# Kernel optimization log

Measured on AMD Instinct MI355X. Metric: run time of the kernel, lower is better.

Reference implementation:

```python
import jax, jax.numpy as jnp
import numpy as np

N = 50000
E = 800000
IN, HID, OUT = 256, 128, 64
NEG_SLOPE = 0.2


def _gat(x, src, dst, W, a_src, a_dst, b, heads, dim, concat):
    # PyG GATConv (eval mode, self-loops already appended to src/dst)
    xh = (x @ W).reshape(N, heads, dim)              # [N,H,D]
    s_src = jnp.einsum('nhd,hd->nh', xh, a_src)       # [N,H]
    s_dst = jnp.einsum('nhd,hd->nh', xh, a_dst)
    e = jax.nn.leaky_relu(s_src[src] + s_dst[dst], NEG_SLOPE)  # [Etot,H]
    m = jax.ops.segment_max(e, dst, num_segments=N)
    e = jnp.exp(e - m[dst])
    z = jax.ops.segment_sum(e, dst, num_segments=N)
    alpha = e / z[dst]                                # segment softmax over incoming edges
    msg = xh[src] * alpha[:, :, None]                 # [Etot,H,D] gather + weight
    out = jax.ops.segment_sum(msg, dst, num_segments=N)  # scatter-add aggregate
    out = out.reshape(N, heads * dim) if concat else out.mean(axis=1)
    return out + b


def setup_inputs():
    key = jax.random.key(0)
    ks = jax.random.split(key, 20)
    sc = 0.05
    inp = {
        'x': jax.random.normal(ks[0], (N, IN), jnp.float32),
        'edge_index': jax.random.randint(ks[1], (2, E), 0, N, jnp.int64) if jax.config.read('jax_enable_x64') else jax.random.randint(ks[1], (2, E), 0, N, jnp.int32),
        # semantic MLP
        'w1': jax.random.normal(ks[2], (IN, HID), jnp.float32) * sc,
        'b1': jnp.zeros((HID,), jnp.float32),
        'w2': jax.random.normal(ks[3], (HID, HID), jnp.float32) * sc,
        'b2': jnp.zeros((HID,), jnp.float32),
        # gat1: HID -> HID//2, heads=4, concat -> 2*HID
        'g1_w': jax.random.normal(ks[4], (HID, 4 * (HID // 2)), jnp.float32) * sc,
        'g1_asrc': jax.random.normal(ks[5], (4, HID // 2), jnp.float32) * sc,
        'g1_adst': jax.random.normal(ks[6], (4, HID // 2), jnp.float32) * sc,
        'g1_b': jnp.zeros((2 * HID,), jnp.float32),
        # gat2: 2*HID -> OUT, heads=2, mean
        'g2_w': jax.random.normal(ks[7], (2 * HID, 2 * OUT), jnp.float32) * sc,
        'g2_asrc': jax.random.normal(ks[8], (2, OUT), jnp.float32) * sc,
        'g2_adst': jax.random.normal(ks[9], (2, OUT), jnp.float32) * sc,
        'g2_b': jnp.zeros((OUT,), jnp.float32),
        # gat3: OUT -> OUT, heads=1, mean
        'g3_w': jax.random.normal(ks[10], (OUT, OUT), jnp.float32) * sc,
        'g3_asrc': jax.random.normal(ks[11], (1, OUT), jnp.float32) * sc,
        'g3_adst': jax.random.normal(ks[12], (1, OUT), jnp.float32) * sc,
        'g3_b': jnp.zeros((OUT,), jnp.float32),
    }
    return inp


def reference(x, edge_index, w1, b1, w2, b2,
              g1_w, g1_asrc, g1_adst, g1_b,
              g2_w, g2_asrc, g2_adst, g2_b,
              g3_w, g3_asrc, g3_adst, g3_b):
    # add self loops once (PyG GATConv default add_self_loops=True)
    loop = jnp.arange(N, dtype=edge_index.dtype)
    src = jnp.concatenate([edge_index[0], loop])
    dst = jnp.concatenate([edge_index[1], loop])
    # semantic MLP (eval: dropout is identity)
    h = jax.nn.relu(x @ w1 + b1)
    h = jax.nn.relu(h @ w2 + b2)
    h = jax.nn.elu(_gat(h, src, dst, g1_w, g1_asrc, g1_adst, g1_b, 4, HID // 2, True))
    h = jax.nn.elu(_gat(h, src, dst, g2_w, g2_asrc, g2_adst, g2_b, 2, OUT, False))
    h = _gat(h, src, dst, g3_w, g3_asrc, g3_adst, g3_b, 1, OUT, False)
    return h
```

## Files before the change

kernel.cpp:

```cpp
#include <hip/hip_runtime.h>
#include <hip/hip_fp16.h>
#include <math.h>

#define NN 50000
#define NE 800000

static inline int ceil_div_h(int a, int b) { return (a + b - 1) / b; }

typedef _Float16 half8 __attribute__((ext_vector_type(8)));
typedef float f32x4 __attribute__((ext_vector_type(4)));

__global__ __launch_bounds__(256)
void prep_kernel(const float* __restrict__ w1, const float* __restrict__ w2,
                 const float* __restrict__ g1w, const float* __restrict__ g2w,
                 const float* __restrict__ g3w, __half* __restrict__ wt,
                 int* __restrict__ cursor) {
  int idx = blockIdx.x * 256 + threadIdx.x;
  if (idx < NN) cursor[idx] = 0;
  const float* W; int K, N, li;
  if (idx < 32768)        { W = w1;  K = 256; N = 128; li = idx; }
  else if (idx < 49152)   { W = w2;  K = 128; N = 128; li = idx - 32768; }
  else if (idx < 81920)   { W = g1w; K = 128; N = 256; li = idx - 49152; }
  else if (idx < 114688)  { W = g2w; K = 256; N = 128; li = idx - 81920; }
  else if (idx < 118784)  { W = g3w; K = 64;  N = 64;  li = idx - 114688; }
  else return;
  int n = li / K, k = li - n * K;
  wt[idx] = __float2half_rn(W[(size_t)k * N + n]);
}

__global__ __launch_bounds__(256)
void mlp_gat1_fused(const float* __restrict__ x,
                    const __half* __restrict__ wt1,
                    const float* __restrict__ b1,
                    const __half* __restrict__ wt2,
                    const float* __restrict__ b2,
                    const __half* __restrict__ wtg1,
                    const float* __restrict__ a_src, const float* __restrict__ a_dst,
                    __half* __restrict__ xh1,
                    float* __restrict__ s_src, float* __restrict__ s_dst) {
  constexpr int SA = 40;
  constexpr int SH = 136;
  __shared__ __align__(16) _Float16 As[64 * SA];
  __shared__ __align__(16) _Float16 Bs[256 * SA];
  __shared__ __align__(16) _Float16 h1s[64 * SH];
  __shared__ __align__(16) _Float16 h2s[64 * SH];
  const int tid = threadIdx.x;
  const int bm = blockIdx.x * 64;
  const int wave = tid >> 6, lane = tid & 63;
  const int l16 = lane & 15, quad = lane >> 4;
  const int wm = (wave & 1) * 32;
  const int wn = (wave >> 1) * 64;

  {
    f32x4 acc[2][4] = {};
    for (int k0 = 0; k0 < 256; k0 += 32) {
      #pragma unroll
      for (int i = 0; i < 2; ++i) {
        int idx = tid + i * 256;
        int m = idx >> 3, q = idx & 7;
        int gm = bm + m;
        float4 v = make_float4(0.f, 0.f, 0.f, 0.f);
        if (gm < NN) v = *(const float4*)&x[(size_t)gm * 256 + k0 + q * 4];
        union { __half2 h2[2]; float2 f2; } u;
        u.h2[0] = __floats2half2_rn(v.x, v.y);
        u.h2[1] = __floats2half2_rn(v.z, v.w);
        *(float2*)&As[m * SA + q * 4] = u.f2;
      }
      #pragma unroll
      for (int i = 0; i < 2; ++i) {
        int idx = tid + i * 256;
        int n = idx >> 2, kq = (idx & 3) * 8;
        *(float4*)&Bs[n * SA + kq] = *(const float4*)&wt1[(size_t)n * 256 + k0 + kq];
      }
      __syncthreads();
      half8 af[2], bf[4];
      #pragma unroll
      for (int mi = 0; mi < 2; ++mi)
        af[mi] = *(const half8*)&As[(wm + mi * 16 + l16) * SA + quad * 8];
      #pragma unroll
      for (int ni = 0; ni < 4; ++ni)
        bf[ni] = *(const half8*)&Bs[(wn + ni * 16 + l16) * SA + quad * 8];
      #pragma unroll
      for (int mi = 0; mi < 2; ++mi)
        #pragma unroll
        for (int ni = 0; ni < 4; ++ni)
          acc[mi][ni] = __builtin_amdgcn_mfma_f32_16x16x32_f16(af[mi], bf[ni], acc[mi][ni], 0, 0, 0);
      __syncthreads();
    }
    #pragma unroll
    for (int mi = 0; mi < 2; ++mi)
      #pragma unroll
      for (int r = 0; r < 4; ++r) {
        int row = wm + mi * 16 + quad * 4 + r;
        #pragma unroll
        for (int ni = 0; ni < 4; ++ni) {
          int col = wn + ni * 16 + l16;
          float v = acc[mi][ni][r] + b1[col];
          v = fmaxf(v, 0.f);
          h1s[row * SH + col] = (_Float16)v;
        }
      }
  }
  __syncthreads();

  {
    f32x4 acc[2][4] = {};
    for (int k0 = 0; k0 < 128; k0 += 32) {
      #pragma unroll
      for (int i = 0; i < 2; ++i) {
        int idx = tid + i * 256;
        int n = idx >> 2, kq = (idx & 3) * 8;
        *(float4*)&Bs[n * SA + kq] = *(const float4*)&wt2[(size_t)n * 128 + k0 + kq];
      }
      __syncthreads();
      half8 af[2], bf[4];
      #pragma unroll
      for (int mi = 0; mi < 2; ++mi)
        af[mi] = *(const half8*)&h1s[(wm + mi * 16 + l16) * SH + k0 + quad * 8];
      #pragma unroll
      for (int ni = 0; ni < 4; ++ni)
        bf[ni] = *(const half8*)&Bs[(wn + ni * 16 + l16) * SA + quad * 8];
      #pragma unroll
      for (int mi = 0; mi < 2; ++mi)
        #pragma unroll
        for (int ni = 0; ni < 4; ++ni)
          acc[mi][ni] = __builtin_amdgcn_mfma_f32_16x16x32_f16(af[mi], bf[ni], acc[mi][ni], 0, 0, 0);
      __syncthreads();
    }
    #pragma unroll
    for (int mi = 0; mi < 2; ++mi)
      #pragma unroll
      for (int r = 0; r < 4; ++r) {
        int row = wm + mi * 16 + quad * 4 + r;
        #pragma unroll
        for (int ni = 0; ni < 4; ++ni) {
          int col = wn + ni * 16 + l16;
          float v = acc[mi][ni][r] + b2[col];
          v = fmaxf(v, 0.f);
          h2s[row * SH + col] = (_Float16)v;
        }
      }
  }
  __syncthreads();

  {
    f32x4 acc[4][4] = {};
    const int wn3 = wave * 64;
    for (int k0 = 0; k0 < 128; k0 += 32) {
      #pragma unroll
      for (int i = 0; i < 4; ++i) {
        int idx = tid + i * 256;
        int n = idx >> 2, kq = (idx & 3) * 8;
        *(float4*)&Bs[n * SA + kq] = *(const float4*)&wtg1[(size_t)n * 128 + k0 + kq];
      }
      __syncthreads();
      half8 af[4], bf[4];
      #pragma unroll
      for (int mi = 0; mi < 4; ++mi)
        af[mi] = *(const half8*)&h2s[(mi * 16 + l16) * SH + k0 + quad * 8];
      #pragma unroll
      for (int ni = 0; ni < 4; ++ni)
        bf[ni] = *(const half8*)&Bs[(wn3 + ni * 16 + l16) * SA + quad * 8];
      #pragma unroll
      for (int mi = 0; mi < 4; ++mi)
        #pragma unroll
        for (int ni = 0; ni < 4; ++ni)
          acc[mi][ni] = __builtin_amdgcn_mfma_f32_16x16x32_f16(af[mi], bf[ni], acc[mi][ni], 0, 0, 0);
      __syncthreads();
    }
    float asv[4], adv[4];
    #pragma unroll
    for (int ni = 0; ni < 4; ++ni) {
      int d = ni * 16 + l16;
      asv[ni] = a_src[wave * 64 + d];
      adv[ni] = a_dst[wave * 64 + d];
    }
    #pragma unroll
    for (int mi = 0; mi < 4; ++mi) {
      #pragma unroll
      for (int r = 0; r < 4; ++r) {
        int gm = bm + mi * 16 + quad * 4 + r;
        float ss = 0.f, sd = 0.f;
        #pragma unroll
        for (int ni = 0; ni < 4; ++ni) {
          float v = acc[mi][ni][r];
          ss = fmaf(v, asv[ni], ss);
          sd = fmaf(v, adv[ni], sd);
          if (gm < NN) xh1[(size_t)gm * 256 + wn3 + ni * 16 + l16] = __float2half_rn(v);
        }
        #pragma unroll
        for (int off = 1; off < 16; off <<= 1) {
          ss += __shfl_xor(ss, off, 64);
          sd += __shfl_xor(sd, off, 64);
        }
        if (l16 == 0 && gm < NN) {
          s_src[gm * 4 + wave] = ss;
          s_dst[gm * 4 + wave] = sd;
        }
      }
    }
  }
}

template<int BM, int TN, int WR, int WC, int ACT, int OUTH, int AF32, int HS>
__global__ __launch_bounds__(256)
void mfma_gemm(const void* __restrict__ Av, const __half* __restrict__ Bt,
               const float* __restrict__ bias, void* __restrict__ Cv,
               const float* __restrict__ a_src, const float* __restrict__ a_dst,
               float* __restrict__ s_src, float* __restrict__ s_dst,
               int M, int N, int K) {
  constexpr int FM = BM / WR / 16;
  constexpr int FN = TN / WC / 16;
  constexpr int SA = 40;
  __shared__ __align__(16) _Float16 As[BM * SA];
  __shared__ __align__(16) _Float16 Bs[TN * SA];
  const int tid = threadIdx.x;
  const int bm = blockIdx.y * BM, bn = blockIdx.x * TN;
  const int wave = tid >> 6, lane = tid & 63;
  const int wm = (wave % WR) * (BM / WR);
  const int wn = (wave / WR) * (TN / WC);
  const int l16 = lane & 15, quad = lane >> 4;

  f32x4 acc[FM][FN] = {};

  for (int k0 = 0; k0 < K; k0 += 32) {
    if (AF32) {
      const float* A = (const float*)Av;
      #pragma unroll
      for (int i = 0; i < (BM * 8) / 256; ++i) {
        int idx = tid + i * 256;
        int m = idx >> 3, q = idx & 7;
        int gm = bm + m;
        float4 v = make_float4(0.f, 0.f, 0.f, 0.f);
        if (gm < M) v = *(const float4*)&A[(size_t)gm * K + k0 + q * 4];
        union { __half2 h2[2]; float2 f2; } u;
        u.h2[0] = __floats2half2_rn(v.x, v.y);
        u.h2[1] = __floats2half2_rn(v.z, v.w);
        *(float2*)&As[m * SA + q * 4] = u.f2;
      }
    } else {
      const __half* A = (const __half*)Av;
      #pragma unroll
      for (int i = 0; i < (BM * 4) / 256; ++i) {
        int idx = tid + i * 256;
        int m = idx >> 2, q = (idx & 3) * 8;
        int gm = bm + m;
        float4 raw = make_float4(0.f, 0.f, 0.f, 0.f);
        if (gm < M) raw = *(const float4*)&A[(size_t)gm * K + k0 + q];
        *(float4*)&As[m * SA + q] = raw;
      }
    }
    #pragma unroll
    for (int i = 0; i < (TN * 4) / 256; ++i) {
      int idx = tid + i * 256;
      int n = idx >> 2, kq = (idx & 3) * 8;
      float4 raw = *(const float4*)&Bt[(size_t)(bn + n) * K + k0 + kq];
      *(float4*)&Bs[n * SA + kq] = raw;
    }
    __syncthreads();
    half8 af[FM], bf[FN];
    #pragma unroll
    for (int mi = 0; mi < FM; ++mi)
      af[mi] = *(const half8*)&As[(wm + mi * 16 + l16) * SA + quad * 8];
    #pragma unroll
    for (int ni = 0; ni < FN; ++ni)
      bf[ni] = *(const half8*)&Bs[(wn + ni * 16 + l16) * SA + quad * 8];
    #pragma unroll
    for (int mi = 0; mi < FM; ++mi)
      #pragma unroll
      for (int ni = 0; ni < FN; ++ni)
        acc[mi][ni] = __builtin_amdgcn_mfma_f32_16x16x32_f16(af[mi], bf[ni], acc[mi][ni], 0, 0, 0);
    __syncthreads();
  }

  #pragma unroll
  for (int mi = 0; mi < FM; ++mi) {
    #pragma unroll
    for (int r = 0; r < 4; ++r) {
      int gm = bm + wm + mi * 16 + quad * 4 + r;
      if (gm >= M) continue;
      #pragma unroll
      for (int ni = 0; ni < FN; ++ni) {
        int gn = bn + wn + ni * 16 + l16;
        float v = acc[mi][ni][r];
        if (bias) v += bias[gn];
        if (ACT == 1) v = fmaxf(v, 0.f);
        if (OUTH) ((__half*)Cv)[(size_t)gm * N + gn] = __float2half_rn(v);
        else      ((float*)Cv)[(size_t)gm * N + gn] = v;
      }
    }
  }

  if (HS > 0) {
    const int h = (bn + wn) >> 6;
    float asv[FN], adv[FN];
    #pragma unroll
    for (int ni = 0; ni < FN; ++ni) {
      int d = ni * 16 + l16;
      asv[ni] = a_src[h * 64 + d];
      adv[ni] = a_dst[h * 64 + d];
    }
    #pragma unroll
    for (int mi = 0; mi < FM; ++mi) {
      #pragma unroll
      for (int r = 0; r < 4; ++r) {
        float ss = 0.f, sd = 0.f;
        #pragma unroll
        for (int ni = 0; ni < FN; ++ni) {
          float v = acc[mi][ni][r];
          ss = fmaf(v, asv[ni], ss);
          sd = fmaf(v, adv[ni], sd);
        }
        #pragma unroll
        for (int off = 1; off < 16; off <<= 1) {
          ss += __shfl_xor(ss, off, 64);
          sd += __shfl_xor(sd, off, 64);
        }
        int gm = bm + wm + mi * 16 + quad * 4 + r;
        if (l16 == 0 && gm < M) {
          s_src[gm * HS + h] = ss;
          s_dst[gm * HS + h] = sd;
        }
      }
    }
  }
}


__global__ __launch_bounds__(256)
void hist_kernel(const int* __restrict__ ei, int* __restrict__ cnt) {
  int e = blockIdx.x * blockDim.x + threadIdx.x;
  if (e >= NE) return;
  atomicAdd(&cnt[ei[NE + e]], 1);
}

__global__ __launch_bounds__(256)
void scan1_kernel(const int* __restrict__ in, int* __restrict__ out,
                  int* __restrict__ bsum, int n) {
  __shared__ int tmp[256];
  int t = threadIdx.x;
  int i = blockIdx.x * 256 + t;
  int v = (i < n) ? in[i] : 0;
  tmp[t] = v;
  __syncthreads();
  for (int off = 1; off < 256; off <<= 1) {
    int u = (t >= off) ? tmp[t - off] : 0;
    __syncthreads();
    tmp[t] += u;
    __syncthreads();
  }
  if (i <= n) out[i] = tmp[t] - v;
  if (t == 255) bsum[blockIdx.x] = tmp[255];
}

__global__ __launch_bounds__(256)
void scan2_kernel(int* __restrict__ data, int n) {
  __shared__ int tmp[256];
  int t = threadIdx.x;
  int v = (t < n) ? data[t] : 0;
  tmp[t] = v;
  __syncthreads();
  for (int off = 1; off < 256; off <<= 1) {
    int u = (t >= off) ? tmp[t - off] : 0;
    __syncthreads();
    tmp[t] += u;
    __syncthreads();
  }
  if (t < n) data[t] = tmp[t] - v;
}

__global__ __launch_bounds__(256)
void scan3_kernel(int* __restrict__ out, const int* __restrict__ bsum,
                  int* __restrict__ cursor, int n) {
  int i = blockIdx.x * 256 + threadIdx.x;
  if (i > n) return;
  int v = out[i] + bsum[blockIdx.x];
  out[i] = v;
  if (i < n) cursor[i] = v;
}

__global__ __launch_bounds__(256)
void scatter_kernel(const int* __restrict__ ei, int* __restrict__ cursor,
                    int* __restrict__ srcs) {
  int e = blockIdx.x * blockDim.x + threadIdx.x;
  if (e >= NE) return;
  int s = ei[e], d = ei[NE + e];
  int pos = atomicAdd(&cursor[d], 1);
  srcs[pos] = s;
}

template<int H, int MODE>
__global__ __launch_bounds__(256)
void gat_aggregate(const int* __restrict__ rowptr, const int* __restrict__ srcs,
                   const float* __restrict__ ssrc, const float* __restrict__ sdst,
                   const __half* __restrict__ xh, const float* __restrict__ bias,
                   void* __restrict__ outv) {
  constexpr int HD = H * 64;
  __shared__ float wbuf[4][64 * H];
  __shared__ int sbuf[4][64];
  const int wslot = threadIdx.x >> 6;
  const int wid = (blockIdx.x * blockDim.x + threadIdx.x) >> 6;
  const int lane = threadIdx.x & 63;
  if (wid >= NN) return;
  const int n = wid;
  const int start = rowptr[n];
  const int end = rowptr[n + 1];
  const int h = (lane * H) >> 6;

  float sdv[H];
  #pragma unroll
  for (int hh = 0; hh < H; ++hh) sdv[hh] = sdst[n * H + hh];

  float z;
  float acc[H];
  {
    float wself[H];
    #pragma unroll
    for (int hh = 0; hh < H; ++hh) {
      float e = ssrc[n * H + hh] + sdv[hh];
      e = e >= 0.f ? e : 0.2f * e;
      wself[hh] = __expf(e);
    }
    float ws = wself[h];
    z = ws;
    const __half* xr = xh + (size_t)n * HD + lane * H;
    if (H == 4) {
      float2 raw = *(const float2*)xr;
      __half2 p0 = *(__half2*)&raw.x;
      __half2 p1 = *(__half2*)&raw.y;
      float2 f0 = __half22float2(p0), f1 = __half22float2(p1);
      acc[0] = ws * f0.x; acc[1] = ws * f0.y; acc[2] = ws * f1.x; acc[3] = ws * f1.y;
    } else if (H == 2) {
      float2 f0 = __half22float2(*(const __half2*)xr);
      acc[0] = ws * f0.x; acc[1] = ws * f0.y;
    } else {
      acc[0] = ws * __half2float(xr[0]);
    }
  }

  for (int base = start; base < end; base += 64) {
    int cnt = end - base;
    if (cnt > 64) cnt = 64;
    if (lane < cnt) {
      int s = srcs[base + lane];
      sbuf[wslot][lane] = s;
      float ev[H];
      if (H == 4) {
        float4 t = *(const float4*)&ssrc[s * 4];
        ev[0] = t.x; ev[1] = t.y; ev[2] = t.z; ev[3] = t.w;
      } else if (H == 2) {
        float2 t = *(const float2*)&ssrc[s * 2];
        ev[0] = t.x; ev[1] = t.y;
      } else {
        ev[0] = ssrc[s];
      }
      #pragma unroll
      for (int hh = 0; hh < H; ++hh) {
        float e = ev[hh] + sdv[hh];
        e = e >= 0.f ? e : 0.2f * e;
        wbuf[wslot][lane * H + hh] = __expf(e);
      }
    }
    #pragma unroll 4
    for (int j = 0; j < cnt; ++j) {
      int s = sbuf[wslot][j];
      float w = wbuf[wslot][j * H + h];
      z += w;
      const __half* xr = xh + (size_t)s * HD + lane * H;
      if (H == 4) {
        float2 raw = *(const float2*)xr;
        __half2 p0 = *(__half2*)&raw.x;
        __half2 p1 = *(__half2*)&raw.y;
        float2 f0 = __half22float2(p0), f1 = __half22float2(p1);
        acc[0] = fmaf(w, f0.x, acc[0]); acc[1] = fmaf(w, f0.y, acc[1]);
        acc[2] = fmaf(w, f1.x, acc[2]); acc[3] = fmaf(w, f1.y, acc[3]);
      } else if (H == 2) {
        float2 f0 = __half22float2(*(const __half2*)xr);
        acc[0] = fmaf(w, f0.x, acc[0]); acc[1] = fmaf(w, f0.y, acc[1]);
      } else {
        acc[0] = fmaf(w, __half2float(xr[0]), acc[0]);
      }
    }
  }
  const float inv = 1.f / z;

  if (MODE == 0) {
    __half* out = (__half*)outv;
    float v[4];
    #pragma unroll
    for (int i = 0; i < 4; ++i) {
      v[i] = acc[i] * inv + bias[lane * 4 + i];
      v[i] = v[i] > 0.f ? v[i] : expm1f(v[i]);
    }
    union { __half2 h2[2]; float2 f2; } u;
    u.h2[0] = __floats2half2_rn(v[0], v[1]);
    u.h2[1] = __floats2half2_rn(v[2], v[3]);
    *(float2*)&out[(size_t)n * 256 + lane * 4] = u.f2;
  } else if (MODE == 1) {
    __half* out = (__half*)outv;
    float sv[2];
    #pragma unroll
    for (int i = 0; i < 2; ++i) {
      float mine = acc[i] * inv;
      float other = __shfl_xor(mine, 32, 64);
      sv[i] = (mine + other) * 0.5f;
    }
    if (lane < 32) {
      float v0 = sv[0] + bias[lane * 2 + 0];
      float v1 = sv[1] + bias[lane * 2 + 1];
      v0 = v0 > 0.f ? v0 : expm1f(v0);
      v1 = v1 > 0.f ? v1 : expm1f(v1);
      *(__half2*)&out[(size_t)n * 64 + lane * 2] = __floats2half2_rn(v0, v1);
    }
  } else {
    float* out = (float*)outv;
    out[(size_t)n * 64 + lane] = acc[0] * inv + bias[lane];
  }
}


extern "C" void kernel_launch(void* const* d_in, const int* in_sizes, int n_in,
                              void* d_out, int out_size, void* d_ws, size_t ws_size,
                              hipStream_t stream) {
  const float* x    = (const float*)d_in[0];
  const int*   ei   = (const int*)d_in[1];
  const float* w1   = (const float*)d_in[2];
  const float* b1   = (const float*)d_in[3];
  const float* w2   = (const float*)d_in[4];
  const float* b2   = (const float*)d_in[5];
  const float* g1w  = (const float*)d_in[6];
  const float* g1as = (const float*)d_in[7];
  const float* g1ad = (const float*)d_in[8];
  const float* g1b  = (const float*)d_in[9];
  const float* g2w  = (const float*)d_in[10];
  const float* g2as = (const float*)d_in[11];
  const float* g2ad = (const float*)d_in[12];
  const float* g2b  = (const float*)d_in[13];
  const float* g3w  = (const float*)d_in[14];
  const float* g3as = (const float*)d_in[15];
  const float* g3ad = (const float*)d_in[16];
  const float* g3b  = (const float*)d_in[17];
  float* out = (float*)d_out;

  float* ws   = (float*)d_ws;
  float* bufA = ws;
  float* bufB = bufA + (size_t)NN * 256;
  float* bufC = bufB + (size_t)NN * 256;
  float* ssrc = bufC + (size_t)NN * 256;
  float* sdst = ssrc + (size_t)NN * 4;
  int* rowptr = (int*)(sdst + (size_t)NN * 4);
  int* cursor = rowptr + (NN + 1);
  int* bsum   = cursor + NN;
  int* srcs   = bsum + 256;
  __half* wt   = (__half*)(srcs + NE);
  __half* wt1  = wt;
  __half* wt2  = wt + 32768;
  __half* wtg1 = wt + 49152;
  __half* wtg2 = wt + 81920;
  __half* wtg3 = wt + 114688;

  __half* xh1 = (__half*)bufC;
  __half* a1  = (__half*)bufA;
  __half* xh2 = (__half*)bufB;
  __half* a2  = (__half*)bufC;
  __half* xh3 = (__half*)bufB;

  const int TB = 256;
  const int grid_m = ceil_div_h(NN, 64);
  const int egrid = ceil_div_h(NE, TB);
  const int sgrid = ceil_div_h(NN + 1, TB);
  const int wgrid = ceil_div_h(NN, 4);

  prep_kernel<<<ceil_div_h(118784, TB), TB, 0, stream>>>(w1, w2, g1w, g2w, g3w, wt, cursor);

  hist_kernel<<<egrid, TB, 0, stream>>>(ei, cursor);
  scan1_kernel<<<sgrid, TB, 0, stream>>>(cursor, rowptr, bsum, NN);
  scan2_kernel<<<1, TB, 0, stream>>>(bsum, sgrid);
  scan3_kernel<<<sgrid, TB, 0, stream>>>(rowptr, bsum, cursor, NN);
  scatter_kernel<<<egrid, TB, 0, stream>>>(ei, cursor, srcs);

  mlp_gat1_fused<<<grid_m, TB, 0, stream>>>(x, wt1, b1, wt2, b2, wtg1,
                                            g1as, g1ad, xh1, ssrc, sdst);
  gat_aggregate<4, 0><<<wgrid, TB, 0, stream>>>(rowptr, srcs, ssrc, sdst, xh1, g1b, a1);

  mfma_gemm<64, 128, 2, 2, 0, 1, 0, 2><<<dim3(1, grid_m), TB, 0, stream>>>(
      a1, wtg2, nullptr, xh2, g2as, g2ad, ssrc, sdst, NN, 128, 256);
  gat_aggregate<2, 1><<<wgrid, TB, 0, stream>>>(rowptr, srcs, ssrc, sdst, xh2, g2b, a2);

  mfma_gemm<64, 64, 4, 1, 0, 1, 0, 1><<<dim3(1, grid_m), TB, 0, stream>>>(
      a2, wtg3, nullptr, xh3, g3as, g3ad, ssrc, sdst, NN, 64, 64);
  gat_aggregate<1, 2><<<wgrid, TB, 0, stream>>>(rowptr, srcs, ssrc, sdst, xh3, g3b, out);
}
```

Baseline: 407.1 us.

## Fuse CSR build and weight prep into one cooperative kernel with grid syncs

Replaces the separate prep, histogram, three-pass scan and scatter launches with a single cooperative kernel of 196 blocks that uses grid.sync between phases. This removes five kernel launches and their inter-kernel gaps. In exchange, the edge-parallel atomic phases now run on far fewer blocks with grid-stride loops, and the cooperative launch adds its own overhead. The fused MLP kernel also reuses one shared-memory region for the B tiles, cutting its LDS footprint, which may raise occupancy.

```diff
diff --git a/kernel.cpp b/kernel.cpp
--- a/kernel.cpp
+++ b/kernel.cpp
@@ -1,31 +1,89 @@
 #include <hip/hip_runtime.h>
 #include <hip/hip_fp16.h>
+#include <hip/hip_cooperative_groups.h>
 #include <math.h>
 
 #define NN 50000
 #define NE 800000
 
+namespace cg = cooperative_groups;
+
 static inline int ceil_div_h(int a, int b) { return (a + b - 1) / b; }
 
 typedef _Float16 half8 __attribute__((ext_vector_type(8)));
 typedef float f32x4 __attribute__((ext_vector_type(4)));
 
 __global__ __launch_bounds__(256)
-void prep_kernel(const float* __restrict__ w1, const float* __restrict__ w2,
-                 const float* __restrict__ g1w, const float* __restrict__ g2w,
-                 const float* __restrict__ g3w, __half* __restrict__ wt,
-                 int* __restrict__ cursor) {
-  int idx = blockIdx.x * 256 + threadIdx.x;
-  if (idx < NN) cursor[idx] = 0;
-  const float* W; int K, N, li;
-  if (idx < 32768)        { W = w1;  K = 256; N = 128; li = idx; }
-  else if (idx < 49152)   { W = w2;  K = 128; N = 128; li = idx - 32768; }
-  else if (idx < 81920)   { W = g1w; K = 128; N = 256; li = idx - 49152; }
-  else if (idx < 114688)  { W = g2w; K = 256; N = 128; li = idx - 81920; }
-  else if (idx < 118784)  { W = g3w; K = 64;  N = 64;  li = idx - 114688; }
-  else return;
-  int n = li / K, k = li - n * K;
-  wt[idx] = __float2half_rn(W[(size_t)k * N + n]);
+void build_all_kernel(const float* __restrict__ w1, const float* __restrict__ w2,
+                      const float* __restrict__ g1w, const float* __restrict__ g2w,
+                      const float* __restrict__ g3w, __half* __restrict__ wt,
+                      const int* __restrict__ ei, int* __restrict__ cursor,
+                      int* __restrict__ rowptr, int* __restrict__ bsum,
+                      int* __restrict__ srcs) {
+  cg::grid_group grid = cg::this_grid();
+  const int tid = threadIdx.x;
+  const int gidx = blockIdx.x * 256 + tid;
+  const int gsz = gridDim.x * 256;
+  __shared__ int tmp[256];
+
+  if (gidx < NN) cursor[gidx] = 0;
+  for (int idx = gidx; idx < 118784; idx += gsz) {
+    const float* W; int K, N, li;
+    if (idx < 32768)        { W = w1;  K = 256; N = 128; li = idx; }
+    else if (idx < 49152)   { W = w2;  K = 128; N = 128; li = idx - 32768; }
+    else if (idx < 81920)   { W = g1w; K = 128; N = 256; li = idx - 49152; }
+    else if (idx < 114688)  { W = g2w; K = 256; N = 128; li = idx - 81920; }
+    else                    { W = g3w; K = 64;  N = 64;  li = idx - 114688; }
+    int n = li / K, k = li - n * K;
+    wt[idx] = __float2half_rn(W[(size_t)k * N + n]);
+  }
+  grid.sync();
+
+  for (int e = gidx; e < NE; e += gsz)
+    atomicAdd(&cursor[ei[NE + e]], 1);
+  grid.sync();
+
+  {
+    int v = (gidx < NN) ? cursor[gidx] : 0;
+    tmp[tid] = v;
+    __syncthreads();
+    for (int off = 1; off < 256; off <<= 1) {
+      int u = (tid >= off) ? tmp[tid - off] : 0;
+      __syncthreads();
+      tmp[tid] += u;
+      __syncthreads();
+    }
+    if (gidx <= NN) rowptr[gidx] = tmp[tid] - v;
+    if (tid == 255) bsum[blockIdx.x] = tmp[255];
+  }
+  grid.sync();
+
+  if (blockIdx.x == 0) {
+    int b = (tid < (int)gridDim.x) ? bsum[tid] : 0;
+    tmp[tid] = b;
+    __syncthreads();
+    for (int off = 1; off < 256; off <<= 1) {
+      int u = (tid >= off) ? tmp[tid - off] : 0;
+      __syncthreads();
+      tmp[tid] += u;
+      __syncthreads();
+    }
+    if (tid < (int)gridDim.x) bsum[tid] = tmp[tid] - b;
+  }
+  grid.sync();
+
+  if (gidx <= NN) {
+    int val = rowptr[gidx] + bsum[blockIdx.x];
+    rowptr[gidx] = val;
+    if (gidx < NN) cursor[gidx] = val;
+  }
+  grid.sync();
+
+  for (int e = gidx; e < NE; e += gsz) {
+    int s = ei[e], d = ei[NE + e];
+    int pos = atomicAdd(&cursor[d], 1);
+    srcs[pos] = s;
+  }
 }
 
 __global__ __launch_bounds__(256)
@@ -40,10 +98,12 @@
                     float* __restrict__ s_src, float* __restrict__ s_dst) {
   constexpr int SA = 40;
   constexpr int SH = 136;
-  __shared__ __align__(16) _Float16 As[64 * SA];
-  __shared__ __align__(16) _Float16 Bs[256 * SA];
-  __shared__ __align__(16) _Float16 h1s[64 * SH];
-  __shared__ __align__(16) _Float16 h2s[64 * SH];
+  __shared__ __align__(16) _Float16 smem[25088];
+  _Float16* As   = smem;
+  _Float16* Bs12 = smem + 2560;
+  _Float16* h1s  = smem + 7680;
+  _Float16* h2s  = smem + 16384;
+  _Float16* Bs3  = Bs12;
   const int tid = threadIdx.x;
   const int bm = blockIdx.x * 64;
   const int wave = tid >> 6, lane = tid & 63;
@@ -70,7 +130,7 @@
       for (int i = 0; i < 2; ++i) {
         int idx = tid + i * 256;
         int n = idx >> 2, kq = (idx & 3) * 8;
-        *(float4*)&Bs[n * SA + kq] = *(const float4*)&wt1[(size_t)n * 256 + k0 + kq];
+        *(float4*)&Bs12[n * SA + kq] = *(const float4*)&wt1[(size_t)n * 256 + k0 + kq];
       }
       __syncthreads();
       half8 af[2], bf[4];
@@ -79,7 +139,7 @@
         af[mi] = *(const half8*)&As[(wm + mi * 16 + l16) * SA + quad * 8];
       #pragma unroll
       for (int ni = 0; ni < 4; ++ni)
-        bf[ni] = *(const half8*)&Bs[(wn + ni * 16 + l16) * SA + quad * 8];
+        bf[ni] = *(const half8*)&Bs12[(wn + ni * 16 + l16) * SA + quad * 8];
       #pragma unroll
       for (int mi = 0; mi < 2; ++mi)
         #pragma unroll
@@ -110,7 +170,7 @@
       for (int i = 0; i < 2; ++i) {
         int idx = tid + i * 256;
         int n = idx >> 2, kq = (idx & 3) * 8;
-        *(float4*)&Bs[n * SA + kq] = *(const float4*)&wt2[(size_t)n * 128 + k0 + kq];
+        *(float4*)&Bs12[n * SA + kq] = *(const float4*)&wt2[(size_t)n * 128 + k0 + kq];
       }
       __syncthreads();
       half8 af[2], bf[4];
@@ -119,7 +179,7 @@
         af[mi] = *(const half8*)&h1s[(wm + mi * 16 + l16) * SH + k0 + quad * 8];
       #pragma unroll
       for (int ni = 0; ni < 4; ++ni)
-        bf[ni] = *(const half8*)&Bs[(wn + ni * 16 + l16) * SA + quad * 8];
+        bf[ni] = *(const half8*)&Bs12[(wn + ni * 16 + l16) * SA + quad * 8];
       #pragma unroll
       for (int mi = 0; mi < 2; ++mi)
         #pragma unroll
@@ -151,7 +211,7 @@
       for (int i = 0; i < 4; ++i) {
         int idx = tid + i * 256;
         int n = idx >> 2, kq = (idx & 3) * 8;
-        *(float4*)&Bs[n * SA + kq] = *(const float4*)&wtg1[(size_t)n * 128 + k0 + kq];
+        *(float4*)&Bs3[n * SA + kq] = *(const float4*)&wtg1[(size_t)n * 128 + k0 + kq];
       }
       __syncthreads();
       half8 af[4], bf[4];
@@ -160,7 +220,7 @@
         af[mi] = *(const half8*)&h2s[(mi * 16 + l16) * SH + k0 + quad * 8];
       #pragma unroll
       for (int ni = 0; ni < 4; ++ni)
-        bf[ni] = *(const half8*)&Bs[(wn3 + ni * 16 + l16) * SA + quad * 8];
+        bf[ni] = *(const half8*)&Bs3[(wn3 + ni * 16 + l16) * SA + quad * 8];
       #pragma unroll
       for (int mi = 0; mi < 4; ++mi)
         #pragma unroll
@@ -324,69 +384,6 @@
       }
     }
   }
-}
-
-
-__global__ __launch_bounds__(256)
-void hist_kernel(const int* __restrict__ ei, int* __restrict__ cnt) {
-  int e = blockIdx.x * blockDim.x + threadIdx.x;
-  if (e >= NE) return;
-  atomicAdd(&cnt[ei[NE + e]], 1);
-}
-
-__global__ __launch_bounds__(256)
-void scan1_kernel(const int* __restrict__ in, int* __restrict__ out,
-                  int* __restrict__ bsum, int n) {
-  __shared__ int tmp[256];
-  int t = threadIdx.x;
-  int i = blockIdx.x * 256 + t;
-  int v = (i < n) ? in[i] : 0;
-  tmp[t] = v;
-  __syncthreads();
-  for (int off = 1; off < 256; off <<= 1) {
-    int u = (t >= off) ? tmp[t - off] : 0;
-    __syncthreads();
-    tmp[t] += u;
-    __syncthreads();
-  }
-  if (i <= n) out[i] = tmp[t] - v;
-  if (t == 255) bsum[blockIdx.x] = tmp[255];
-}
-
-__global__ __launch_bounds__(256)
-void scan2_kernel(int* __restrict__ data, int n) {
-  __shared__ int tmp[256];
-  int t = threadIdx.x;
-  int v = (t < n) ? data[t] : 0;
-  tmp[t] = v;
-  __syncthreads();
-  for (int off = 1; off < 256; off <<= 1) {
-    int u = (t >= off) ? tmp[t - off] : 0;
-    __syncthreads();
-    tmp[t] += u;
-    __syncthreads();
-  }
-  if (t < n) data[t] = tmp[t] - v;
-}
-
-__global__ __launch_bounds__(256)
-void scan3_kernel(int* __restrict__ out, const int* __restrict__ bsum,
-                  int* __restrict__ cursor, int n) {
-  int i = blockIdx.x * 256 + threadIdx.x;
-  if (i > n) return;
-  int v = out[i] + bsum[blockIdx.x];
-  out[i] = v;
-  if (i < n) cursor[i] = v;
-}
-
-__global__ __launch_bounds__(256)
-void scatter_kernel(const int* __restrict__ ei, int* __restrict__ cursor,
-                    int* __restrict__ srcs) {
-  int e = blockIdx.x * blockDim.x + threadIdx.x;
-  if (e >= NE) return;
-  int s = ei[e], d = ei[NE + e];
-  int pos = atomicAdd(&cursor[d], 1);
-  srcs[pos] = s;
 }
 
 template<int H, int MODE>
@@ -567,17 +564,15 @@
 
   const int TB = 256;
   const int grid_m = ceil_div_h(NN, 64);
-  const int egrid = ceil_div_h(NE, TB);
-  const int sgrid = ceil_div_h(NN + 1, TB);
   const int wgrid = ceil_div_h(NN, 4);
 
-  prep_kernel<<<ceil_div_h(118784, TB), TB, 0, stream>>>(w1, w2, g1w, g2w, g3w, wt, cursor);
-
-  hist_kernel<<<egrid, TB, 0, stream>>>(ei, cursor);
-  scan1_kernel<<<sgrid, TB, 0, stream>>>(cursor, rowptr, bsum, NN);
-  scan2_kernel<<<1, TB, 0, stream>>>(bsum, sgrid);
-  scan3_kernel<<<sgrid, TB, 0, stream>>>(rowptr, bsum, cursor, NN);
-  scatter_kernel<<<egrid, TB, 0, stream>>>(ei, cursor, srcs);
+  {
+    void* args[] = {(void*)&w1, (void*)&w2, (void*)&g1w, (void*)&g2w, (void*)&g3w,
+                    (void*)&wt, (void*)&ei, (void*)&cursor, (void*)&rowptr,
+                    (void*)&bsum, (void*)&srcs};
+    hipLaunchCooperativeKernel((void*)build_all_kernel, dim3(196), dim3(TB),
+                               args, 0, stream);
+  }
 
   mlp_gat1_fused<<<grid_m, TB, 0, stream>>>(x, wt1, b1, wt2, b2, wtg1,
                                             g1as, g1ad, xh1, ssrc, sdst);
```

Result: slower. 531.4 us (+30.5%).
